# Performance work log

Measured on AMD Instinct MI355X. Metric: run time of the kernel, lower is better.

The kernel has to match this reference:

```python
import jax, jax.numpy as jnp
import numpy as np

D_MODEL = 1024
N_HEADS = 16
D_HEAD = 64


def setup_inputs() -> dict:
    key = jax.random.key(0)
    ks = jax.random.split(key, 5)
    B, T = 2, 2048
    scale = 1.0 / np.sqrt(D_MODEL)
    x = jax.random.normal(ks[0], (B, T, D_MODEL), dtype=jnp.float32)
    Wq = jax.random.normal(ks[1], (N_HEADS * D_HEAD, D_MODEL), dtype=jnp.float32) * scale
    Wk = jax.random.normal(ks[2], (N_HEADS * D_HEAD, D_MODEL), dtype=jnp.float32) * scale
    Wv = jax.random.normal(ks[3], (N_HEADS * D_HEAD, D_MODEL), dtype=jnp.float32) * scale
    Wo = jax.random.normal(ks[4], (D_MODEL, N_HEADS * D_HEAD), dtype=jnp.float32) * scale
    return {"x": x, "Wq": Wq, "Wk": Wk, "Wv": Wv, "Wo": Wo}


def reference(x, Wq, Wk, Wv, Wo):
    B, T, D = x.shape
    # Linear(y = x @ W.T), then split heads: [B, H, T, d]
    def split_heads(y):
        return y.reshape(B, T, N_HEADS, D_HEAD).transpose(0, 2, 1, 3)
    q = split_heads(x @ Wq.T)
    k = split_heads(x @ Wk.T)
    v = split_heads(x @ Wv.T)
    scale = D_HEAD ** -0.5
    # Materialized [B, H, T, T] scores, as in the original module
    scores = jnp.einsum('bhtd,bhTd->bhtT', q, k) * scale
    attn = jax.nn.softmax(scores, axis=-1)
    y = jnp.einsum('bhtT,bhTd->bhtd', attn, v)
    y = y.transpose(0, 2, 1, 3).reshape(B, T, N_HEADS * D_HEAD)
    return y @ Wo.T
```

## Files before the change

kernel.cpp:

```cpp
#include <hip/hip_runtime.h>
#include <hip/hip_bf16.h>

typedef __attribute__((ext_vector_type(8))) short bf16x8;
typedef __attribute__((ext_vector_type(4))) float f32x4;
typedef unsigned short u16t;

#define DEVINL static __device__ __forceinline__

DEVINL u16t f2bf(float f) {
  union { __hip_bfloat16 h; u16t u; } cv;
  cv.h = __float2bfloat16(f);
  return cv.u;
}

DEVINL unsigned cvt_pk_bf16(float a, float b) {
  unsigned r;
  asm("v_cvt_pk_bf16_f32 %0, %1, %2" : "=v"(r) : "v"(a), "v"(b));
  return r;
}

DEVINL void async16(void* lds, const void* g) {
  __builtin_amdgcn_global_load_lds((const __attribute__((address_space(1))) void*)g,
                                   (__attribute__((address_space(3))) void*)lds,
                                   16, 0, 0);
}

__global__ __launch_bounds__(256) void convert_bf16(
    const float* __restrict__ x,  const float* __restrict__ wq,
    const float* __restrict__ wk, const float* __restrict__ wv,
    const float* __restrict__ wo,
    u16t* __restrict__ xb, u16t* __restrict__ wqb, u16t* __restrict__ wkb,
    u16t* __restrict__ wvb, u16t* __restrict__ wob) {
  const int blk = blockIdx.x;
  const float* src; u16t* dst; size_t off;
  if (blk < 4096)      { src = x;  dst = xb;  off = (size_t)blk * 1024; }
  else if (blk < 5120) { src = wq; dst = wqb; off = (size_t)(blk - 4096) * 1024; }
  else if (blk < 6144) { src = wk; dst = wkb; off = (size_t)(blk - 5120) * 1024; }
  else if (blk < 7168) { src = wv; dst = wvb; off = (size_t)(blk - 6144) * 1024; }
  else                 { src = wo; dst = wob; off = (size_t)(blk - 7168) * 1024; }
  const size_t i = off + (size_t)threadIdx.x * 4;
  const float4 v = *(const float4*)&src[i];
  ushort4 r;
  r.x = f2bf(v.x); r.y = f2bf(v.y); r.z = f2bf(v.z); r.w = f2bf(v.w);
  *(ushort4*)&dst[i] = r;
}

template <int MODE>
__global__ __launch_bounds__(256) void gemm_bt(
    const u16t* __restrict__ A, const u16t* __restrict__ B,
    void* __restrict__ C0, void* __restrict__ C1, void* __restrict__ C2,
    int M, int N, int K) {
  __shared__ u16t As[2][128 * 32];
  __shared__ u16t Bs[2][128 * 32];

  const int tid = threadIdx.x;
  const int lane = tid & 63;
  const int w = tid >> 6;
  const int wm = w >> 1, wn = w & 1;
  const int quad = lane >> 4, cl = lane & 15;
  const int m0 = blockIdx.y * 128;
  const int n0 = blockIdx.x * 128;

  const int srow = lane >> 2;
  const int scol = (lane & 3) * 8;

  f32x4 acc[4][4] = {};

  for (int k0 = 0; k0 < K; k0 += 64) {
    __syncthreads();
    #pragma unroll
    for (int p = 0; p < 2; ++p)
      #pragma unroll
      for (int ii = 0; ii < 2; ++ii) {
        const int c = w + ii * 4;
        async16(&As[p][c * 512], &A[(size_t)(m0 + c * 16 + srow) * K + k0 + p * 32 + scol]);
        async16(&Bs[p][c * 512], &B[(size_t)(n0 + c * 16 + srow) * K + k0 + p * 32 + scol]);
      }
    __syncthreads();
    #pragma unroll
    for (int p = 0; p < 2; ++p) {
      bf16x8 af[4], bfr[4];
      #pragma unroll
      for (int i = 0; i < 4; ++i)
        af[i] = *(const bf16x8*)&As[p][(wm * 64 + i * 16 + cl) * 32 + quad * 8];
      #pragma unroll
      for (int j = 0; j < 4; ++j)
        bfr[j] = *(const bf16x8*)&Bs[p][(wn * 64 + j * 16 + cl) * 32 + quad * 8];
      #pragma unroll
      for (int i = 0; i < 4; ++i)
        #pragma unroll
        for (int j = 0; j < 4; ++j)
          acc[i][j] = __builtin_amdgcn_mfma_f32_16x16x32_bf16(af[i], bfr[j], acc[i][j], 0, 0, 0);
    }
  }

  const int nz = n0 >> 10;
  #pragma unroll
  for (int i = 0; i < 4; ++i)
    #pragma unroll
    for (int j = 0; j < 4; ++j) {
      const int mb = m0 + wm * 64 + i * 16 + quad * 4;
      const int n  = n0 + wn * 64 + j * 16 + cl;
      if (MODE == 0) {
        #pragma unroll
        for (int r = 0; r < 4; ++r)
          ((float*)C0)[(size_t)(mb + r) * N + n] = acc[i][j][r];
      } else {
        const int nw = n & 1023, h = nw >> 6, d = nw & 63;
        const int b = mb >> 11, tb = mb & 2047;
        const size_t bh = (size_t)(b * 16 + h);
        if (nz == 2) {
          ushort4 v4;
          v4.x = f2bf(acc[i][j][0]); v4.y = f2bf(acc[i][j][1]);
          v4.z = f2bf(acc[i][j][2]); v4.w = f2bf(acc[i][j][3]);
          const size_t addr = (bh << 17) +
              (size_t)(((d >> 4) * 256 + (tb >> 3)) * 128 + (d & 15) * 8 + (tb & 7));
          *(ushort4*)&((u16t*)C2)[addr] = v4;
        } else if (nz == 1) {
          const size_t basea = (bh << 17) +
              (size_t)(((tb >> 4) * 8 + (d >> 3)) * 128 + (d & 7));
          #pragma unroll
          for (int r = 0; r < 4; ++r)
            ((u16t*)C1)[basea + ((tb & 15) + r) * 8] = f2bf(acc[i][j][r]);
        } else {
          #pragma unroll
          for (int r = 0; r < 4; ++r)
            ((u16t*)C0)[(bh * 2048 + tb + r) * 64 + d] =
                f2bf(acc[i][j][r] * 0.18033688011112043f);
        }
      }
    }
}

__global__ __launch_bounds__(256) void flash_attn(
    const u16t* __restrict__ Q, const u16t* __restrict__ Kt,
    const u16t* __restrict__ Vt, u16t* __restrict__ Y) {
  __shared__ u16t Ps[4 * 16 * 136];

  const int tid = threadIdx.x;
  const int lane = tid & 63;
  const int w = tid >> 6;
  const int quad = lane >> 4, cl = lane & 15;
  const int bh = blockIdx.y;
  const int q0 = blockIdx.x * 64;
  const u16t* Kb = Kt + ((size_t)bh << 17);
  const u16t* Vb = Vt + ((size_t)bh << 17);

  bf16x8 aq[2];
  #pragma unroll
  for (int ks = 0; ks < 2; ++ks)
    aq[ks] = *(const bf16x8*)&Q[((size_t)bh * 2048 + q0 + w * 16 + cl) * 64 + ks * 32 + quad * 8];

  bf16x8 onesf;
  #pragma unroll
  for (int i = 0; i < 8; ++i) onesf[i] = (short)0x3F80;

  f32x4 o[4] = {};
  f32x4 psum = {};

  u16t* Pw = &Ps[w * 16 * 136];

  for (int jt = 0; jt < 16; ++jt) {
    const int j0 = jt * 128;

    f32x4 s[8] = {};
    #pragma unroll
    for (int ks = 0; ks < 2; ++ks) {
      bf16x8 kf[8];
      #pragma unroll
      for (int js = 0; js < 8; ++js)
        kf[js] = *(const bf16x8*)&Kb[(size_t)((((j0 >> 4) + js) * 8 + ks * 4) * 128) + lane * 8];
      #pragma unroll
      for (int js = 0; js < 8; ++js)
        s[js] = __builtin_amdgcn_mfma_f32_16x16x32_bf16(kf[js], aq[ks], s[js], 0, 0, 0);
    }

    #pragma unroll
    for (int js = 0; js < 8; ++js) {
      uint2 pk;
      pk.x = cvt_pk_bf16(__builtin_exp2f(s[js][0]), __builtin_exp2f(s[js][1]));
      pk.y = cvt_pk_bf16(__builtin_exp2f(s[js][2]), __builtin_exp2f(s[js][3]));
      *(uint2*)&Pw[cl * 136 + js * 16 + quad * 4] = pk;
    }

    #pragma unroll
    for (int ks = 0; ks < 4; ++ks) {
      const bf16x8 ap = *(const bf16x8*)&Pw[cl * 136 + ks * 32 + quad * 8];
      bf16x8 vf[4];
      #pragma unroll
      for (int ds = 0; ds < 4; ++ds)
        vf[ds] = *(const bf16x8*)&Vb[(size_t)((ds * 256 + (j0 >> 3) + ks * 4) * 128) + lane * 8];
      psum = __builtin_amdgcn_mfma_f32_16x16x32_bf16(ap, onesf, psum, 0, 0, 0);
      #pragma unroll
      for (int ds = 0; ds < 4; ++ds)
        o[ds] = __builtin_amdgcn_mfma_f32_16x16x32_bf16(ap, vf[ds], o[ds], 0, 0, 0);
    }
  }

  float inv[4];
  #pragma unroll
  for (int r = 0; r < 4; ++r) inv[r] = __builtin_amdgcn_rcpf(psum[r]);

  const int b = bh >> 4, h = bh & 15;
  #pragma unroll
  for (int ds = 0; ds < 4; ++ds)
    #pragma unroll
    for (int r = 0; r < 4; ++r) {
      const int t = q0 + w * 16 + quad * 4 + r;
      const int d = ds * 16 + cl;
      Y[((size_t)b * 2048 + t) * 1024 + h * 64 + d] = f2bf(o[ds][r] * inv[r]);
    }
}

extern "C" void kernel_launch(void* const* d_in, const int* in_sizes, int n_in,
                              void* d_out, int out_size, void* d_ws, size_t ws_size,
                              hipStream_t stream) {
  (void)in_sizes; (void)n_in; (void)out_size; (void)ws_size;
  const float* x  = (const float*)d_in[0];
  const float* Wq = (const float*)d_in[1];
  const float* Wk = (const float*)d_in[2];
  const float* Wv = (const float*)d_in[3];
  const float* Wo = (const float*)d_in[4];

  char* ws = (char*)d_ws;
  const size_t MB = 1024 * 1024;
  u16t* xb  = (u16t*)(ws);
  u16t* Wqb = (u16t*)(ws + 8 * MB);
  u16t* Wkb = (u16t*)(ws + 10 * MB);
  u16t* Wvb = (u16t*)(ws + 12 * MB);
  u16t* Wob = (u16t*)(ws + 14 * MB);
  u16t* Qw  = (u16t*)(ws + 16 * MB);
  u16t* Ktw = (u16t*)(ws + 24 * MB);
  u16t* Vtw = (u16t*)(ws + 32 * MB);
  u16t* Yw  = xb;

  convert_bf16<<<8192, 256, 0, stream>>>(x, Wq, Wk, Wv, Wo, xb, Wqb, Wkb, Wvb, Wob);
  gemm_bt<1><<<dim3(24, 32), 256, 0, stream>>>(
      xb, Wqb, Qw, Ktw, Vtw, 4096, 3072, 1024);
  flash_attn<<<dim3(32, 32), 256, 0, stream>>>(Qw, Ktw, Vtw, Yw);
  gemm_bt<0><<<dim3(8, 32), 256, 0, stream>>>(
      Yw, Wob, d_out, d_out, d_out, 4096, 1024, 1024);
}
```

Measured before the change: 208.6 us.

## Feed P to PV MFMA directly from registers using 16x16x16 layout

```diff
diff --git a/kernel.cpp b/kernel.cpp
--- a/kernel.cpp
+++ b/kernel.cpp
@@ -2,6 +2,7 @@
 #include <hip/hip_bf16.h>
 
 typedef __attribute__((ext_vector_type(8))) short bf16x8;
+typedef __attribute__((ext_vector_type(4))) short bf16x4;
 typedef __attribute__((ext_vector_type(4))) float f32x4;
 typedef unsigned short u16t;
 
@@ -17,6 +18,15 @@
   unsigned r;
   asm("v_cvt_pk_bf16_f32 %0, %1, %2" : "=v"(r) : "v"(a), "v"(b));
   return r;
+}
+
+DEVINL f32x4 mfma16(bf16x4 a, bf16x4 b, f32x4 c) {
+#if __has_builtin(__builtin_amdgcn_mfma_f32_16x16x16bf16_1k)
+  return __builtin_amdgcn_mfma_f32_16x16x16bf16_1k(a, b, c, 0, 0, 0);
+#else
+  asm("v_mfma_f32_16x16x16_bf16 %0, %1, %2, %0" : "+v"(c) : "v"(a), "v"(b));
+  return c;
+#endif
 }
 
 DEVINL void async16(void* lds, const void* g) {
@@ -113,8 +123,7 @@
           ushort4 v4;
           v4.x = f2bf(acc[i][j][0]); v4.y = f2bf(acc[i][j][1]);
           v4.z = f2bf(acc[i][j][2]); v4.w = f2bf(acc[i][j][3]);
-          const size_t addr = (bh << 17) +
-              (size_t)(((d >> 4) * 256 + (tb >> 3)) * 128 + (d & 15) * 8 + (tb & 7));
+          const size_t addr = (bh << 17) + (size_t)((tb >> 2) * 256 + d * 4);
           *(ushort4*)&((u16t*)C2)[addr] = v4;
         } else if (nz == 1) {
           const size_t basea = (bh << 17) +
@@ -132,34 +141,28 @@
     }
 }
 
-__global__ __launch_bounds__(256) void flash_attn(
+__global__ __launch_bounds__(64) void flash_attn(
     const u16t* __restrict__ Q, const u16t* __restrict__ Kt,
     const u16t* __restrict__ Vt, u16t* __restrict__ Y) {
-  __shared__ u16t Ps[4 * 16 * 136];
-
-  const int tid = threadIdx.x;
-  const int lane = tid & 63;
-  const int w = tid >> 6;
+  const int lane = threadIdx.x & 63;
   const int quad = lane >> 4, cl = lane & 15;
   const int bh = blockIdx.y;
-  const int q0 = blockIdx.x * 64;
+  const int q0 = blockIdx.x * 16;
   const u16t* Kb = Kt + ((size_t)bh << 17);
   const u16t* Vb = Vt + ((size_t)bh << 17);
 
   bf16x8 aq[2];
   #pragma unroll
   for (int ks = 0; ks < 2; ++ks)
-    aq[ks] = *(const bf16x8*)&Q[((size_t)bh * 2048 + q0 + w * 16 + cl) * 64 + ks * 32 + quad * 8];
-
-  bf16x8 onesf;
-  #pragma unroll
-  for (int i = 0; i < 8; ++i) onesf[i] = (short)0x3F80;
+    aq[ks] = *(const bf16x8*)&Q[((size_t)bh * 2048 + q0 + cl) * 64 + ks * 32 + quad * 8];
+
+  bf16x4 ones4;
+  #pragma unroll
+  for (int i = 0; i < 4; ++i) ones4[i] = (short)0x3F80;
 
   f32x4 o[4] = {};
   f32x4 psum = {};
 
-  u16t* Pw = &Ps[w * 16 * 136];
-
   for (int jt = 0; jt < 16; ++jt) {
     const int j0 = jt * 128;
 
@@ -175,25 +178,24 @@
         s[js] = __builtin_amdgcn_mfma_f32_16x16x32_bf16(kf[js], aq[ks], s[js], 0, 0, 0);
     }
 
+    bf16x4 ap[8];
     #pragma unroll
     for (int js = 0; js < 8; ++js) {
-      uint2 pk;
-      pk.x = cvt_pk_bf16(__builtin_exp2f(s[js][0]), __builtin_exp2f(s[js][1]));
-      pk.y = cvt_pk_bf16(__builtin_exp2f(s[js][2]), __builtin_exp2f(s[js][3]));
-      *(uint2*)&Pw[cl * 136 + js * 16 + quad * 4] = pk;
-    }
-
-    #pragma unroll
-    for (int ks = 0; ks < 4; ++ks) {
-      const bf16x8 ap = *(const bf16x8*)&Pw[cl * 136 + ks * 32 + quad * 8];
-      bf16x8 vf[4];
-      #pragma unroll
-      for (int ds = 0; ds < 4; ++ds)
-        vf[ds] = *(const bf16x8*)&Vb[(size_t)((ds * 256 + (j0 >> 3) + ks * 4) * 128) + lane * 8];
-      psum = __builtin_amdgcn_mfma_f32_16x16x32_bf16(ap, onesf, psum, 0, 0, 0);
-      #pragma unroll
-      for (int ds = 0; ds < 4; ++ds)
-        o[ds] = __builtin_amdgcn_mfma_f32_16x16x32_bf16(ap, vf[ds], o[ds], 0, 0, 0);
+      union { unsigned u[2]; bf16x4 v; } pk;
+      pk.u[0] = cvt_pk_bf16(__builtin_exp2f(s[js][0]), __builtin_exp2f(s[js][1]));
+      pk.u[1] = cvt_pk_bf16(__builtin_exp2f(s[js][2]), __builtin_exp2f(s[js][3]));
+      ap[js] = pk.v;
+    }
+
+    #pragma unroll
+    for (int js = 0; js < 8; ++js) {
+      psum = mfma16(ap[js], ones4, psum);
+      const int vbase = ((j0 >> 2) + js * 4 + quad) * 256 + cl * 4;
+      #pragma unroll
+      for (int ds = 0; ds < 4; ++ds) {
+        const bf16x4 vf = *(const bf16x4*)&Vb[(size_t)(vbase + ds * 64)];
+        o[ds] = mfma16(ap[js], vf, o[ds]);
+      }
     }
   }
 
@@ -206,7 +208,7 @@
   for (int ds = 0; ds < 4; ++ds)
     #pragma unroll
     for (int r = 0; r < 4; ++r) {
-      const int t = q0 + w * 16 + quad * 4 + r;
+      const int t = q0 + quad * 4 + r;
       const int d = ds * 16 + cl;
       Y[((size_t)b * 2048 + t) * 1024 + h * 64 + d] = f2bf(o[ds][r] * inv[r]);
     }
@@ -237,7 +239,7 @@
   convert_bf16<<<8192, 256, 0, stream>>>(x, Wq, Wk, Wv, Wo, xb, Wqb, Wkb, Wvb, Wob);
   gemm_bt<1><<<dim3(24, 32), 256, 0, stream>>>(
       xb, Wqb, Qw, Ktw, Vtw, 4096, 3072, 1024);
-  flash_attn<<<dim3(32, 32), 256, 0, stream>>>(Qw, Ktw, Vtw, Yw);
+  flash_attn<<<dim3(128, 32), 64, 0, stream>>>(Qw, Ktw, Vtw, Yw);
   gemm_bt<0><<<dim3(8, 32), 256, 0, stream>>>(
       Yw, Wob, d_out, d_out, d_out, 4096, 1024, 1024);
 }
```

After: 309.6 us. +48.4%, slower.
